# Kernel optimization log

Measured on AMD Instinct MI355X. Metric: run time of the kernel, lower is better.

## Reference

```python
import jax, jax.numpy as jnp
import numpy as np
from jax import lax

D_MODEL = 768
D_STATE = 64
D_CONV = 4
EXPAND = 2
HEADDIM = 64
D_INNER = EXPAND * D_MODEL          # 1536
NHEADS = D_INNER // HEADDIM          # 24
NGROUPS = 1
CONV_DIM = D_INNER + 2 * NGROUPS * D_STATE      # 1664
D_IN_PROJ = 2 * D_INNER + 2 * NGROUPS * D_STATE + NHEADS  # 3224
EPS = 1e-5


def setup_inputs() -> dict:
    key = jax.random.key(0)
    ks = jax.random.split(key, 8)
    B, L = 2, 4096
    x = jax.random.normal(ks[0], (B, L, D_MODEL), jnp.float32)
    W_in = jax.random.normal(ks[1], (D_MODEL, D_IN_PROJ), jnp.float32) * (D_MODEL ** -0.5)
    conv_w = jax.random.normal(ks[2], (CONV_DIM, D_CONV), jnp.float32) * 0.2
    conv_b = jnp.zeros((CONV_DIM,), jnp.float32)
    # dt_bias so that softplus(dt_bias) ~ [1e-3, 1e-1], like mamba init
    dt = jax.random.uniform(ks[3], (NHEADS,), jnp.float32, 1e-3, 1e-1)
    dt_bias = dt + jnp.log(-jnp.expm1(-dt))
    A_log = jnp.log(jax.random.uniform(ks[4], (NHEADS,), jnp.float32, 1.0, 16.0))
    D = jnp.ones((NHEADS,), jnp.float32)
    norm_w = jnp.ones((D_INNER,), jnp.float32)
    W_out = jax.random.normal(ks[5], (D_INNER, D_MODEL), jnp.float32) * (D_INNER ** -0.5)
    return {"x": x, "W_in": W_in, "conv_w": conv_w, "conv_b": conv_b,
            "dt_bias": dt_bias, "A_log": A_log, "D": D,
            "norm_w": norm_w, "W_out": W_out}


def _mamba2(x, W_in, conv_w, conv_b, dt_bias, A_log, D, norm_w, W_out):
    B, L, _ = x.shape
    zxbcdt = x @ W_in                                  # (B,L,3224)
    z = zxbcdt[..., :D_INNER]                          # gate
    xBC = zxbcdt[..., D_INNER:D_INNER + CONV_DIM]
    dt = zxbcdt[..., D_INNER + CONV_DIM:]              # (B,L,H)
    dt = jax.nn.softplus(dt + dt_bias)

    # causal depthwise conv1d, kernel D_CONV, then SiLU
    xp = jnp.pad(xBC, ((0, 0), (D_CONV - 1, 0), (0, 0)))
    conv = sum(xp[:, k:k + L, :] * conv_w[:, k] for k in range(D_CONV))
    xBC = jax.nn.silu(conv + conv_b)

    xs = xBC[..., :D_INNER].reshape(B, L, NHEADS, HEADDIM)
    Bm = xBC[..., D_INNER:D_INNER + D_STATE]           # (B,L,N)
    Cm = xBC[..., D_INNER + D_STATE:]                  # (B,L,N)

    A = -jnp.exp(A_log)                                # (H,)
    dA = jnp.exp(dt * A)                               # (B,L,H)

    def step(h, inp):
        dA_t, dt_t, x_t, B_t, C_t = inp
        # h: (B,H,P,N)
        h = h * dA_t[:, :, None, None] \
            + (dt_t[:, :, None] * x_t)[..., None] * B_t[:, None, None, :]
        y = jnp.einsum('bhpn,bn->bhp', h, C_t)
        return h, y

    inps = (jnp.moveaxis(dA, 1, 0), jnp.moveaxis(dt, 1, 0),
            jnp.moveaxis(xs, 1, 0), jnp.moveaxis(Bm, 1, 0),
            jnp.moveaxis(Cm, 1, 0))
    h0 = jnp.zeros((B, NHEADS, HEADDIM, D_STATE), x.dtype)
    _, ys = lax.scan(step, h0, inps)                   # (L,B,H,P)
    y = jnp.moveaxis(ys, 0, 1) + D[None, None, :, None] * xs
    y = y.reshape(B, L, D_INNER)

    # gated RMSNorm: norm(y * silu(z)) * norm_w
    y = y * jax.nn.silu(z)
    y = y * lax.rsqrt(jnp.mean(y * y, axis=-1, keepdims=True) + EPS) * norm_w
    return y @ W_out


def reference(x, W_in, conv_w, conv_b, dt_bias, A_log, D, norm_w, W_out):
    return _mamba2(x, W_in, conv_w, conv_b, dt_bias, A_log, D, norm_w, W_out)
```

## Files before the change

### kernel.cpp

```cpp
#include <hip/hip_runtime.h>

#define B_   2
#define L_   4096
#define DM   768
#define DI   1536
#define DS   64
#define H_   24
#define P_   64
#define CD   1664
#define NPJ  3224
#define N1   3200
#define Q_   64
#define NC   64
#define SP   76
#define HS   72
#define WDS  772
#define CROWS 16

typedef short          bf16x8 __attribute__((ext_vector_type(8)));
typedef _Float16       f16x8  __attribute__((ext_vector_type(8)));
typedef _Float16       f16x4  __attribute__((ext_vector_type(4)));
typedef unsigned short us8    __attribute__((ext_vector_type(8)));
typedef unsigned short us4    __attribute__((ext_vector_type(4)));
typedef float          f32x4  __attribute__((ext_vector_type(4)));

__device__ __forceinline__ unsigned short f2bf(float f) {
  unsigned u = __float_as_uint(f);
  u += 0x7fffu + ((u >> 16) & 1u);
  return (unsigned short)(u >> 16);
}
__device__ __forceinline__ float bf2f(unsigned short u) {
  return __uint_as_float(((unsigned)u) << 16);
}
__device__ __forceinline__ float siluf(float x) { return x / (1.f + expf(-x)); }
__device__ __forceinline__ float softplusf(float x) { return (x > 20.f) ? x : log1pf(expf(x)); }

__device__ __forceinline__ void gload16(const unsigned short* g, unsigned short* l) {
  __builtin_amdgcn_global_load_lds(
      (const __attribute__((address_space(1))) void*)g,
      (__attribute__((address_space(3))) void*)l, 16, 0, 0);
}

__global__ __launch_bounds__(256)
void k_transpose_cast(const float* __restrict__ src, unsigned short* __restrict__ dst,
                      int R, int C)
{
  __shared__ float tile[32][33];
  const int tx = threadIdx.x & 31, ty = threadIdx.x >> 5;
  const int r0 = blockIdx.x * 32, c0 = blockIdx.y * 32;
#pragma unroll
  for (int r = 0; r < 4; ++r) {
    int rr = r0 + ty + r * 8, cc = c0 + tx;
    if (rr < R && cc < C) tile[ty + r * 8][tx] = src[(size_t)rr * C + cc];
  }
  __syncthreads();
#pragma unroll
  for (int r = 0; r < 4; ++r) {
    int orow = c0 + ty + r * 8, ocol = r0 + tx;
    if (orow < C && ocol < R) dst[(size_t)orow * R + ocol] = f2bf(tile[tx][ty + r * 8]);
  }
}

__global__ void k_wdtT(const float* __restrict__ W_in, float* __restrict__ WdtT)
{
  const int idx = blockIdx.x * 256 + threadIdx.x;
  if (idx >= H_ * DM) return;
  const int k = idx / H_, h = idx % H_;
  WdtT[(size_t)h * DM + k] = W_in[(size_t)k * NPJ + N1 + h];
}

template<int BM, int BN, int WM, int WN, bool OUT_BF16>
__global__ __launch_bounds__((BM / WM) * (BN / WN) * 64)
void k_gemm_t(const unsigned short* __restrict__ A, const unsigned short* __restrict__ Bt,
              void* __restrict__ C0v, int ld0, int ncol0,
              void* __restrict__ C1v, int ld1, int K)
{
  constexpr int MI = WM / 16, NI = WN / 16;
  constexpr int WAVES_N = BN / WN;
  constexpr int T  = (BM / WM) * (BN / WN) * 64;
  constexpr int RG = T / 8;
  constexpr int RA = BM / RG, RB = BN / RG;
  const int m0 = blockIdx.x * BM, n0 = blockIdx.y * BN;
  __shared__ unsigned short As[BM][64];
  __shared__ unsigned short Bs[BN][64];
  const int tid  = threadIdx.x;
  const int wave = tid >> 6, lane = tid & 63;
  const int quad = lane >> 4, r16 = lane & 15;
  const int wm = (wave / WAVES_N) * WM, wn = (wave % WAVES_N) * WN;

  const int lr8 = lane >> 3;
  const int csw = ((lane & 7) ^ lr8) * 8;
  const unsigned short* gA = A  + (size_t)(m0 + wave * 8 + lr8) * K + csw;
  const unsigned short* gB = Bt + (size_t)(n0 + wave * 8 + lr8) * K + csw;
  unsigned short* lA = &As[wave * 8][0] + (size_t)lane * 8;
  unsigned short* lB = &Bs[wave * 8][0] + (size_t)lane * 8;

  f32x4 acc[MI][NI];
#pragma unroll
  for (int mi = 0; mi < MI; ++mi)
#pragma unroll
    for (int ni = 0; ni < NI; ++ni) acc[mi][ni] = (f32x4){0.f, 0.f, 0.f, 0.f};

  for (int k0 = 0; k0 < K; k0 += 64) {
#pragma unroll
    for (int r = 0; r < RA; ++r)
      gload16(gA + (size_t)(r * RG) * K + k0, lA + (size_t)r * RG * 64);
#pragma unroll
    for (int r = 0; r < RB; ++r)
      gload16(gB + (size_t)(r * RG) * K + k0, lB + (size_t)r * RG * 64);
    __syncthreads();
    bf16x8 af[MI][2], bfr[NI][2];
#pragma unroll
    for (int mi = 0; mi < MI; ++mi)
#pragma unroll
      for (int ks = 0; ks < 2; ++ks)
        af[mi][ks] = *(const bf16x8*)&As[wm + mi * 16 + r16][((quad + ks * 4) ^ (r16 & 7)) * 8];
#pragma unroll
    for (int ni = 0; ni < NI; ++ni)
#pragma unroll
      for (int ks = 0; ks < 2; ++ks)
        bfr[ni][ks] = *(const bf16x8*)&Bs[wn + ni * 16 + r16][((quad + ks * 4) ^ (r16 & 7)) * 8];
#pragma unroll
    for (int mi = 0; mi < MI; ++mi)
#pragma unroll
      for (int ni = 0; ni < NI; ++ni)
#pragma unroll
        for (int ks = 0; ks < 2; ++ks)
          acc[mi][ni] = __builtin_amdgcn_mfma_f32_16x16x32_bf16(
              af[mi][ks], bfr[ni][ks], acc[mi][ni], 0, 0, 0);
    __syncthreads();
  }
#pragma unroll
  for (int mi = 0; mi < MI; ++mi)
#pragma unroll
    for (int ni = 0; ni < NI; ++ni) {
      int col = n0 + wn + ni * 16 + r16;
      void* dst; int ld, c;
      if (col < ncol0) { dst = C0v; ld = ld0; c = col; }
      else             { dst = C1v; ld = ld1; c = col - ncol0; }
#pragma unroll
      for (int r = 0; r < 4; ++r) {
        int row = m0 + wm + mi * 16 + quad * 4 + r;
        if (OUT_BF16) ((unsigned short*)dst)[(size_t)row * ld + c] = f2bf(acc[mi][ni][r]);
        else          ((float*)dst)[(size_t)row * ld + c] = acc[mi][ni][r];
      }
    }
}

__global__ __launch_bounds__(256)
void k_conv2(const unsigned short* __restrict__ xbc, const float* __restrict__ cw,
             const float* __restrict__ cb, _Float16* __restrict__ xs,
             float* __restrict__ Bm, float* __restrict__ Cm)
{
  const int ch = blockIdx.x * 256 + threadIdx.x;
  if (ch >= CD) return;
  const int r0 = blockIdx.y * CROWS;
  const float w0 = cw[ch * 4], w1 = cw[ch * 4 + 1], w2 = cw[ch * 4 + 2], w3 = cw[ch * 4 + 3];
  const float bias = cb[ch];
  float a, b, c;
  if ((r0 & (L_ - 1)) == 0) {
    a = 0.f; b = 0.f; c = 0.f;
  } else {
    a = bf2f(xbc[(size_t)(r0 - 3) * CD + ch]);
    b = bf2f(xbc[(size_t)(r0 - 2) * CD + ch]);
    c = bf2f(xbc[(size_t)(r0 - 1) * CD + ch]);
  }
#pragma unroll
  for (int i = 0; i < CROWS; ++i) {
    const int lr = r0 + i;
    float d = bf2f(xbc[(size_t)lr * CD + ch]);
    float v = siluf(bias + a * w0 + b * w1 + c * w2 + d * w3);
    a = b; b = c; c = d;
    if (ch < DI)           xs[(size_t)lr * DI + ch] = (_Float16)v;
    else if (ch < DI + DS) Bm[(size_t)lr * DS + (ch - DI)] = v;
    else                   Cm[(size_t)lr * DS + (ch - DI - DS)] = v;
  }
}

__global__ __launch_bounds__(192)
void k_dt2(const float* __restrict__ x, const float* __restrict__ WdtT,
           const float* __restrict__ dt_bias, float* __restrict__ dtv,
           unsigned short* __restrict__ xb)
{
  __shared__ float sW[H_][WDS];
  for (int i = threadIdx.x; i < H_ * DM; i += 192)
    sW[i / DM][i % DM] = WdtT[i];
  const int h = threadIdx.x % H_, rloc = threadIdx.x / H_;
  const int lrow = blockIdx.x * 8 + rloc;
  const float* xr = x + (size_t)lrow * DM;
  __syncthreads();
  float acc = 0.f;
#pragma unroll 8
  for (int k = 0; k < DM; k += 4) {
    f32x4 xv = *(const f32x4*)(xr + k);
    f32x4 wv = *(const f32x4*)&sW[h][k];
    acc += xv[0] * wv[0] + xv[1] * wv[1] + xv[2] * wv[2] + xv[3] * wv[3];
  }
  dtv[(size_t)lrow * H_ + h] = softplusf(acc + dt_bias[h]);
  const float* xi = xr + h * 32;
  unsigned short* xo = xb + (size_t)lrow * DM + h * 32;
#pragma unroll
  for (int j = 0; j < 32; j += 8) {
    f32x4 a = *(const f32x4*)(xi + j);
    f32x4 b = *(const f32x4*)(xi + j + 4);
    us8 o;
#pragma unroll
    for (int e = 0; e < 4; ++e) { o[e] = f2bf(a[e]); o[e + 4] = f2bf(b[e]); }
    *(us8*)(xo + j) = o;
  }
}

__global__ __launch_bounds__(256)
void k_intra(const _Float16* __restrict__ xs, const float* __restrict__ Bm,
             const float* __restrict__ Cm, const float* __restrict__ dtv,
             const float* __restrict__ A_log, const float* __restrict__ Dp,
             float* __restrict__ cumA, _Float16* __restrict__ ytot,
             _Float16* __restrict__ Sbuf)
{
  const int c = blockIdx.x, h = blockIdx.y, bz = blockIdx.z;
  const int gidx = (bz * H_ + h) * NC + c;
  __shared__ _Float16 sCW[Q_][HS];
  __shared__ _Float16 sB [Q_][HS];
  __shared__ _Float16 sBT[Q_][HS];
  __shared__ _Float16 sXT[Q_][HS];
  __shared__ float scum[Q_], sdt[Q_];
  const int tid = threadIdx.x;
  const int rowbase = bz * L_ + c * Q_;

  {
    const int j = tid >> 2, s16 = (tid & 3) * 16;
    if (tid < Q_) {
      const float dtval = dtv[(size_t)(rowbase + tid) * H_ + h];
      sdt[tid] = dtval;
      const float A = -expf(A_log[h]);
      float v = dtval;
#pragma unroll
      for (int off = 1; off < 64; off <<= 1) {
        float o = __shfl_up(v, off, 64);
        if (tid >= off) v += o;
      }
      v *= A;
      scum[tid] = v;
      cumA[(size_t)gidx * Q_ + tid] = v;
    }
    const _Float16* xsrc = xs + (size_t)(rowbase + j) * DI + h * P_ + s16;
    f16x8 xv0 = *(const f16x8*)xsrc;
    f16x8 xv1 = *(const f16x8*)(xsrc + 8);
    f32x4 bv[4], cv[4];
    const float* bsrc = Bm + (size_t)(rowbase + j) * DS + s16;
    const float* csrc = Cm + (size_t)(rowbase + j) * DS + s16;
#pragma unroll
    for (int q = 0; q < 4; ++q) {
      bv[q] = *(const f32x4*)(bsrc + q * 4);
      cv[q] = *(const f32x4*)(csrc + q * 4);
    }
    __syncthreads();
    const float coef = expf(scum[Q_ - 1] - scum[j]) * sdt[j];
    union { f16x8 v; _Float16 e[8]; } pc[2], pb[2];
#pragma unroll
    for (int q = 0; q < 4; ++q)
#pragma unroll
      for (int e = 0; e < 4; ++e) {
        int o = q * 4 + e;
        pc[o >> 3].e[o & 7] = (_Float16)cv[q][e];
        pb[o >> 3].e[o & 7] = (_Float16)bv[q][e];
        sBT[s16 + o][j] = (_Float16)(bv[q][e] * coef);
        sXT[s16 + o][j] = (o < 8) ? xv0[o] : xv1[o - 8];
      }
    *(f16x8*)&sCW[j][s16]     = pc[0].v;
    *(f16x8*)&sCW[j][s16 + 8] = pc[1].v;
    *(f16x8*)&sB [j][s16]     = pb[0].v;
    *(f16x8*)&sB [j][s16 + 8] = pb[1].v;
  }
  __syncthreads();

  const int wave = tid >> 6, lane = tid & 63;
  const int quad = lane >> 4, r16 = lane & 15;
  const int i0 = wave * 16;
  const int irow = i0 + quad * 4;

  f32x4 g[4];
#pragma unroll
  for (int q = 0; q < 4; ++q) g[q] = (f32x4){0.f, 0.f, 0.f, 0.f};
#pragma unroll
  for (int ni = 0; ni < 4; ++ni) {
    if (ni <= wave) {
#pragma unroll
      for (int ks = 0; ks < 2; ++ks)
        g[ni] = __builtin_amdgcn_mfma_f32_16x16x32_f16(
            *(const f16x8*)&sCW[i0 + r16][ks * 32 + quad * 8],
            *(const f16x8*)&sB [ni * 16 + r16][ks * 32 + quad * 8], g[ni], 0, 0, 0);
    }
  }
  float wv[4][4];
#pragma unroll
  for (int ni = 0; ni < 4; ++ni)
#pragma unroll
    for (int r = 0; r < 4; ++r) {
      int i = irow + r, jcol = ni * 16 + r16;
      float v = 0.f;
      if (ni <= wave && jcol <= i)
        v = g[ni][r] * expf(scum[i] - scum[jcol]) * sdt[jcol];
      wv[ni][r] = v;
    }
  __syncthreads();
#pragma unroll
  for (int ni = 0; ni < 4; ++ni)
#pragma unroll
    for (int r = 0; r < 4; ++r)
      sCW[irow + r][ni * 16 + r16] = (_Float16)wv[ni][r];
  __syncthreads();

  const float Dh = Dp[h];
  f32x4 y[4];
#pragma unroll
  for (int q = 0; q < 4; ++q) y[q] = (f32x4){0.f, 0.f, 0.f, 0.f};
#pragma unroll
  for (int ni = 0; ni < 4; ++ni)
#pragma unroll
    for (int ks = 0; ks < 2; ++ks) {
      if (ks == 0 || wave >= 2)
        y[ni] = __builtin_amdgcn_mfma_f32_16x16x32_f16(
            *(const f16x8*)&sCW[i0 + r16][ks * 32 + quad * 8],
            *(const f16x8*)&sXT[ni * 16 + r16][ks * 32 + quad * 8], y[ni], 0, 0, 0);
    }
#pragma unroll
  for (int ni = 0; ni < 4; ++ni)
#pragma unroll
    for (int r = 0; r < 4; ++r) {
      const float xval = (float)sXT[ni * 16 + r16][irow + r];
      ytot[(size_t)(rowbase + irow + r) * DI + h * P_ + ni * 16 + r16] =
          (_Float16)(y[ni][r] + Dh * xval);
    }

  f32x4 t4[4];
#pragma unroll
  for (int q = 0; q < 4; ++q) t4[q] = (f32x4){0.f, 0.f, 0.f, 0.f};
#pragma unroll
  for (int ni = 0; ni < 4; ++ni)
#pragma unroll
    for (int ks = 0; ks < 2; ++ks)
      t4[ni] = __builtin_amdgcn_mfma_f32_16x16x32_f16(
          *(const f16x8*)&sBT[i0 + r16][ks * 32 + quad * 8],
          *(const f16x8*)&sXT[ni * 16 + r16][ks * 32 + quad * 8], t4[ni], 0, 0, 0);
  _Float16* sp = Sbuf + (size_t)gidx * (DS * P_);
#pragma unroll
  for (int ni = 0; ni < 4; ++ni)
#pragma unroll
    for (int r = 0; r < 4; ++r)
      sp[(irow + r) * P_ + ni * 16 + r16] = (_Float16)t4[ni][r];
}

__global__ __launch_bounds__(64)
void k_chunkscan(_Float16* __restrict__ Sbuf, const float* __restrict__ cumA)
{
  const int seg = blockIdx.x, h = blockIdx.y, bz = blockIdx.z;
  const int bh = bz * H_ + h;
  __shared__ float dec[NC];
  const int tid = threadIdx.x;
  dec[tid] = expf(cumA[((size_t)(bh * NC + tid)) * Q_ + (Q_ - 1)]);
  __syncthreads();
  _Float16* base = Sbuf + (size_t)bh * NC * (DS * P_) + (size_t)seg * 256 + (size_t)tid * 4;
  float s[4] = {0.f, 0.f, 0.f, 0.f};
  f16x4 bA[8], bB[8];
#pragma unroll
  for (int j = 0; j < 8; ++j) bA[j] = *(const f16x4*)(base + (size_t)j * (DS * P_));
#pragma unroll
  for (int g = 0; g < 8; ++g) {
    if (g + 1 < 8) {
#pragma unroll
      for (int j = 0; j < 8; ++j) {
        f16x4 v = *(const f16x4*)(base + (size_t)((g + 1) * 8 + j) * (DS * P_));
        if (g & 1) bA[j] = v; else bB[j] = v;
      }
    }
#pragma unroll
    for (int j = 0; j < 8; ++j) {
      const int c = g * 8 + j;
      f16x4 cur = (g & 1) ? bB[j] : bA[j];
      f16x4 sto;
#pragma unroll
      for (int e = 0; e < 4; ++e) sto[e] = (_Float16)s[e];
      *(f16x4*)(base + (size_t)c * (DS * P_)) = sto;
      const float d = dec[c];
#pragma unroll
      for (int e = 0; e < 4; ++e) s[e] = s[e] * d + (float)cur[e];
    }
  }
}

__global__ __launch_bounds__(256)
void k_inter(const float* __restrict__ Cm, const float* __restrict__ cumA,
             const _Float16* __restrict__ Sbuf, _Float16* __restrict__ ytot)
{
  const int c = blockIdx.x, h = blockIdx.y, bz = blockIdx.z;
  const int gidx = (bz * H_ + h) * NC + c;
  __shared__ float sS[DS][SP];
  __shared__ float sC[Q_][SP];
  __shared__ float scum[Q_];
  const int tid = threadIdx.x;
  const int jr = tid >> 2, blk = (tid & 3) * 16;
  const int rowbase = bz * L_ + c * Q_;
  {
    const _Float16* ssrc = Sbuf + (size_t)gidx * (DS * P_) + jr * P_ + blk;
    f16x8 sv0 = *(const f16x8*)ssrc;
    f16x8 sv1 = *(const f16x8*)(ssrc + 8);
    const float* csrc = Cm + (size_t)(rowbase + jr) * DS + blk;
#pragma unroll
    for (int o = 0; o < 8; ++o) {
      sS[jr][blk + o]     = (float)sv0[o];
      sS[jr][blk + 8 + o] = (float)sv1[o];
    }
#pragma unroll
    for (int q = 0; q < 4; ++q)
      *(f32x4*)&sC[jr][blk + q * 4] = *(const f32x4*)(csrc + q * 4);
    if (tid < Q_) scum[tid] = cumA[(size_t)gidx * Q_ + tid];
  }
  __syncthreads();
  const int i = jr;
  f32x4 acc[4];
#pragma unroll
  for (int q = 0; q < 4; ++q) acc[q] = (f32x4){0.f, 0.f, 0.f, 0.f};
  for (int n = 0; n < DS; ++n) {
    float cv = sC[i][n];
#pragma unroll
    for (int q = 0; q < 4; ++q) acc[q] += cv * *(const f32x4*)&sS[n][blk + q * 4];
  }
  const float e = expf(scum[i]);
  _Float16* yt = ytot + (size_t)(rowbase + i) * DI + h * P_ + blk;
  f16x8 y0 = *(const f16x8*)yt;
  f16x8 y1 = *(const f16x8*)(yt + 8);
#pragma unroll
  for (int o = 0; o < 16; ++o) {
    float cur = (float)((o < 8) ? y0[o] : y1[o - 8]);
    cur += e * acc[o >> 2][o & 3];
    if (o < 8) y0[o] = (_Float16)cur; else y1[o - 8] = (_Float16)cur;
  }
  *(f16x8*)yt = y0;
  *(f16x8*)(yt + 8) = y1;
}

__global__ __launch_bounds__(192)
void k_rms(const unsigned short* __restrict__ z, const _Float16* __restrict__ ytot,
           const float* __restrict__ norm_w, unsigned short* __restrict__ ynorm)
{
  const int row = blockIdx.x, tid = threadIdx.x;
  const int e0 = tid * 8;
  us8 zv = *(const us8*)(z + (size_t)row * DI + e0);
  f16x8 yv = *(const f16x8*)(ytot + (size_t)row * DI + e0);
  float g[8];
  float ss = 0.f;
#pragma unroll
  for (int q = 0; q < 8; ++q) {
    g[q] = (float)yv[q] * siluf(bf2f(zv[q]));
    ss += g[q] * g[q];
  }
#pragma unroll
  for (int off = 32; off > 0; off >>= 1) ss += __shfl_down(ss, off);
  __shared__ float wsum[3];
  __shared__ float sscale;
  if ((tid & 63) == 0) wsum[tid >> 6] = ss;
  __syncthreads();
  if (tid == 0) sscale = rsqrtf((wsum[0] + wsum[1] + wsum[2]) * (1.f / DI) + 1e-5f);
  __syncthreads();
  const float sc = sscale;
  us8 o;
#pragma unroll
  for (int q = 0; q < 8; ++q) o[q] = f2bf(g[q] * sc * norm_w[e0 + q]);
  *(us8*)(ynorm + (size_t)row * DI + e0) = o;
}

extern "C" void kernel_launch(void* const* d_in, const int* in_sizes, int n_in,
                              void* d_out, int out_size, void* d_ws, size_t ws_size,
                              hipStream_t stream)
{
  (void)in_sizes; (void)n_in; (void)out_size;
  const float* x       = (const float*)d_in[0];
  const float* W_in    = (const float*)d_in[1];
  const float* conv_w  = (const float*)d_in[2];
  const float* conv_b  = (const float*)d_in[3];
  const float* dt_bias = (const float*)d_in[4];
  const float* A_log   = (const float*)d_in[5];
  const float* Dp      = (const float*)d_in[6];
  const float* norm_w  = (const float*)d_in[7];
  const float* W_out   = (const float*)d_in[8];
  float* out = (float*)d_out;

  const int nb = ((size_t)2 * L_ * 16320 + 7385088 <= ws_size) ? 2 : 1;
  const int rows = nb * L_;

  char* ws = (char*)d_ws;
  unsigned short* zseg = (unsigned short*)ws;  ws += (size_t)rows * DI * 2;
  unsigned short* xbc  = (unsigned short*)ws;  ws += (size_t)rows * CD * 2;
  _Float16* xs   = (_Float16*)ws;  ws += (size_t)rows * DI * 2;
  _Float16* ytot = (_Float16*)ws;  ws += (size_t)rows * DI * 2;
  float* Bm   = (float*)ws;  ws += (size_t)rows * DS * 4;
  float* Cm   = (float*)ws;  ws += (size_t)rows * DS * 4;
  float* dtv  = (float*)ws;  ws += (size_t)rows * H_ * 4;
  float* cumA = (float*)ws;  ws += (size_t)rows * H_ * 4;
  _Float16* Sbuf = (_Float16*)ws;  ws += (size_t)rows * 3072;
  unsigned short* WinT  = (unsigned short*)ws; ws += (size_t)NPJ * DM * 2;
  unsigned short* WoutT = (unsigned short*)ws; ws += (size_t)DM * DI * 2;
  float* WdtT   = (float*)ws;  ws += (size_t)H_ * DM * 4;
  unsigned short* xb    = (unsigned short*)Sbuf;
  unsigned short* ynorm = (unsigned short*)xs;

  k_transpose_cast<<<dim3(24, (NPJ + 31) / 32), 256, 0, stream>>>(W_in, WinT, DM, NPJ);
  k_transpose_cast<<<dim3(48, 24), 256, 0, stream>>>(W_out, WoutT, DI, DM);
  k_wdtT<<<(H_ * DM + 255) / 256, 256, 0, stream>>>(W_in, WdtT);

  for (int b0 = 0; b0 < B_; b0 += nb) {
    const float* xp = x + (size_t)b0 * L_ * DM;

    k_dt2<<<rows / 8, 192, 0, stream>>>(xp, WdtT, dt_bias, dtv, xb);
    k_gemm_t<256, 128, 64, 64, true><<<dim3(rows / 256, N1 / 128), 512, 0, stream>>>(
        xb, WinT, zseg, DI, DI, xbc, CD, DM);
    k_conv2<<<dim3(7, rows / CROWS), 256, 0, stream>>>(xbc, conv_w, conv_b, xs, Bm, Cm);
    k_intra<<<dim3(NC, H_, nb), 256, 0, stream>>>(xs, Bm, Cm, dtv, A_log, Dp, cumA, ytot, Sbuf);
    k_chunkscan<<<dim3(16, H_, nb), 64, 0, stream>>>(Sbuf, cumA);
    k_inter<<<dim3(NC, H_, nb), 256, 0, stream>>>(Cm, cumA, Sbuf, ytot);
    k_rms<<<rows, 192, 0, stream>>>(zseg, ytot, norm_w, ynorm);
    k_gemm_t<128, 64, 64, 32, false><<<dim3(rows / 128, DM / 64), 256, 0, stream>>>(
        ynorm, WoutT, out + (size_t)b0 * L_ * DM, DM, DM, out + (size_t)b0 * L_ * DM, DM, DI);
  }
}
```

Baseline: 326.4 us.

## Restructure dt projection kernel with register tiling over rows and split-K

After: 349.3 us. 7.0% more time.

```diff
diff --git a/kernel.cpp b/kernel.cpp
--- a/kernel.cpp
+++ b/kernel.cpp
@@ -14,7 +14,6 @@
 #define NC   64
 #define SP   76
 #define HS   72
-#define WDS  772
 #define CROWS 16
 
 typedef short          bf16x8 __attribute__((ext_vector_type(8)));
@@ -177,28 +176,51 @@
   }
 }
 
-__global__ __launch_bounds__(192)
+__global__ __launch_bounds__(384)
 void k_dt2(const float* __restrict__ x, const float* __restrict__ WdtT,
            const float* __restrict__ dt_bias, float* __restrict__ dtv,
            unsigned short* __restrict__ xb)
 {
-  __shared__ float sW[H_][WDS];
-  for (int i = threadIdx.x; i < H_ * DM; i += 192)
-    sW[i / DM][i % DM] = WdtT[i];
-  const int h = threadIdx.x % H_, rloc = threadIdx.x / H_;
-  const int lrow = blockIdx.x * 8 + rloc;
-  const float* xr = x + (size_t)lrow * DM;
-  __syncthreads();
-  float acc = 0.f;
-#pragma unroll 8
-  for (int k = 0; k < DM; k += 4) {
-    f32x4 xv = *(const f32x4*)(xr + k);
-    f32x4 wv = *(const f32x4*)&sW[h][k];
-    acc += xv[0] * wv[0] + xv[1] * wv[1] + xv[2] * wv[2] + xv[3] * wv[3];
-  }
-  dtv[(size_t)lrow * H_ + h] = softplusf(acc + dt_bias[h]);
-  const float* xi = xr + h * 32;
-  unsigned short* xo = xb + (size_t)lrow * DM + h * 32;
+  __shared__ float sWf[H_ * 788];
+  const int tid = threadIdx.x;
+  for (int i = tid; i < H_ * DM; i += 384) {
+    const int h = i / DM, k = i % DM;
+    sWf[h * 788 + (k / 192) * 196 + (k % 192)] = WdtT[i];
+  }
+  const int hh = tid >> 2, rg = tid & 3;
+  const int h = hh >> 2, kq = hh & 3;
+  const int row0 = blockIdx.x * 16;
+  const float* xq = x + (size_t)(row0 + rg * 4) * DM + kq * 192;
+  const float* wq = &sWf[h * 788 + kq * 196];
+  __syncthreads();
+  float a0 = 0.f, a1 = 0.f, a2 = 0.f, a3 = 0.f;
+#pragma unroll 4
+  for (int j = 0; j < 192; j += 4) {
+    f32x4 wv = *(const f32x4*)(wq + j);
+    f32x4 x0 = *(const f32x4*)(xq + j);
+    f32x4 x1 = *(const f32x4*)(xq + DM + j);
+    f32x4 x2 = *(const f32x4*)(xq + 2 * DM + j);
+    f32x4 x3 = *(const f32x4*)(xq + 3 * DM + j);
+    a0 += x0[0] * wv[0] + x0[1] * wv[1] + x0[2] * wv[2] + x0[3] * wv[3];
+    a1 += x1[0] * wv[0] + x1[1] * wv[1] + x1[2] * wv[2] + x1[3] * wv[3];
+    a2 += x2[0] * wv[0] + x2[1] * wv[1] + x2[2] * wv[2] + x2[3] * wv[3];
+    a3 += x3[0] * wv[0] + x3[1] * wv[1] + x3[2] * wv[2] + x3[3] * wv[3];
+  }
+  a0 += __shfl_xor(a0, 4); a0 += __shfl_xor(a0, 8);
+  a1 += __shfl_xor(a1, 4); a1 += __shfl_xor(a1, 8);
+  a2 += __shfl_xor(a2, 4); a2 += __shfl_xor(a2, 8);
+  a3 += __shfl_xor(a3, 4); a3 += __shfl_xor(a3, 8);
+  if (kq == 0) {
+    const float bias = dt_bias[h];
+    const int r = row0 + rg * 4;
+    dtv[(size_t)(r + 0) * H_ + h] = softplusf(a0 + bias);
+    dtv[(size_t)(r + 1) * H_ + h] = softplusf(a1 + bias);
+    dtv[(size_t)(r + 2) * H_ + h] = softplusf(a2 + bias);
+    dtv[(size_t)(r + 3) * H_ + h] = softplusf(a3 + bias);
+  }
+  const int crow = tid / 24, ccol = (tid % 24) * 32;
+  const float* xi = x + (size_t)(row0 + crow) * DM + ccol;
+  unsigned short* xo = xb + (size_t)(row0 + crow) * DM + ccol;
 #pragma unroll
   for (int j = 0; j < 32; j += 8) {
     f32x4 a = *(const f32x4*)(xi + j);
@@ -512,7 +534,7 @@
   for (int b0 = 0; b0 < B_; b0 += nb) {
     const float* xp = x + (size_t)b0 * L_ * DM;
 
-    k_dt2<<<rows / 8, 192, 0, stream>>>(xp, WdtT, dt_bias, dtv, xb);
+    k_dt2<<<rows / 16, 384, 0, stream>>>(xp, WdtT, dt_bias, dtv, xb);
     k_gemm_t<256, 128, 64, 64, true><<<dim3(rows / 256, N1 / 128), 512, 0, stream>>>(
         xb, WinT, zseg, DI, DI, xbc, CD, DM);
     k_conv2<<<dim3(7, rows / CROWS), 256, 0, stream>>>(xbc, conv_w, conv_b, xs, Bm, Cm);
```
